# Optimization experiments

Measured on AMD Instinct MI355X. Metric: run time of the kernel, lower is better.

## Reference

```python
import jax, jax.numpy as jnp
import numpy as np

B, T, N, D = 4, 16, 1024, 128
LN_EPS = 1e-5


def setup_inputs() -> dict:
    key = jax.random.key(0)
    k1, k2, k3 = jax.random.split(key, 3)
    X = jax.random.normal(k1, (B, T, N, D), dtype=jnp.float32)
    # normalized adjacency (dense, values in [0,1))
    A = jax.random.uniform(k2, (N, N), dtype=jnp.float32)
    # GCN linear weight (torch nn.Linear, bias=False): out = x @ W.T
    W = jax.random.normal(k3, (D, D), dtype=jnp.float32) / np.sqrt(D)
    gamma = jnp.ones((D,), dtype=jnp.float32)
    beta = jnp.zeros((D,), dtype=jnp.float32)
    return {"X": X, "A": A, "W": W, "gamma": gamma, "beta": beta}


def reference(X, A, W, gamma, beta):
    d = X.shape[-1]
    inv_sqrt_d_a = np.float32(1.0 / np.sqrt(d + 1e-8))  # score scale
    inv_sqrt_d_b = np.float32(1.0 / np.sqrt(d + 1e-9))  # output scale
    # dynamic attention-like scores over nodes: (b,T,N,N)
    scores = jnp.einsum('btnd,btmd->btnm', X, X)
    St = jax.nn.softmax(scores, axis=-1) * inv_sqrt_d_a  # dropout p=0 => identity
    Aeff = A * St                                        # adjacency-masked attention
    # GCN: relu((Aeff @ X) @ W.T)
    h = jnp.einsum('btnm,btmd->btnd', Aeff, X)
    h = jax.nn.relu(h @ W.T) * inv_sqrt_d_b
    # LayerNorm over last dim
    mu = jnp.mean(h, axis=-1, keepdims=True)
    var = jnp.mean(jnp.square(h - mu), axis=-1, keepdims=True)
    h = (h - mu) * jax.lax.rsqrt(var + LN_EPS) * gamma + beta
    # residual
    return h + X
```

## Files before the change

### kernel.cpp

```cpp
#include <hip/hip_runtime.h>


#define NNODES 1024
#define DDIM   128
#define BROWS  128
#define WROWS  16
#define MC     64
#define NCHUNK (NNODES / MC)
#define THREADS 512

#define CA 0.08838834764831845f
#define CB 0.08838834764831845f
#define LN_EPS 1e-5f

typedef __attribute__((ext_vector_type(8))) short bf16x8;
typedef __attribute__((ext_vector_type(4))) float f32x4;
typedef __attribute__((ext_vector_type(2))) unsigned int u32x2;

#define STILE(s) (64*(s))

#define XB0_OFF 0
#define XB1_OFF 8192
#define P_OFF   16384
#define P_S     72
#define H_S     136
#define SM_TOT  25600

#define TRREAD16(T, AP)                                                     \
  asm volatile(                                                             \
    "ds_read_b64_tr_b16 %0, %16 offset:0\n\t"                               \
    "ds_read_b64_tr_b16 %1, %16 offset:128\n\t"                             \
    "ds_read_b64_tr_b16 %2, %16 offset:2048\n\t"                            \
    "ds_read_b64_tr_b16 %3, %16 offset:2176\n\t"                            \
    "ds_read_b64_tr_b16 %4, %16 offset:4096\n\t"                            \
    "ds_read_b64_tr_b16 %5, %16 offset:4224\n\t"                            \
    "ds_read_b64_tr_b16 %6, %16 offset:6144\n\t"                            \
    "ds_read_b64_tr_b16 %7, %16 offset:6272\n\t"                            \
    "ds_read_b64_tr_b16 %8, %16 offset:8192\n\t"                            \
    "ds_read_b64_tr_b16 %9, %16 offset:8320\n\t"                            \
    "ds_read_b64_tr_b16 %10, %16 offset:10240\n\t"                          \
    "ds_read_b64_tr_b16 %11, %16 offset:10368\n\t"                          \
    "ds_read_b64_tr_b16 %12, %16 offset:12288\n\t"                          \
    "ds_read_b64_tr_b16 %13, %16 offset:12416\n\t"                          \
    "ds_read_b64_tr_b16 %14, %16 offset:14336\n\t"                          \
    "ds_read_b64_tr_b16 %15, %16 offset:14464\n\t"                          \
    "s_waitcnt lgkmcnt(0)"                                                  \
    : "=&v"(T[0]), "=&v"(T[1]), "=&v"(T[2]), "=&v"(T[3]),                   \
      "=&v"(T[4]), "=&v"(T[5]), "=&v"(T[6]), "=&v"(T[7]),                   \
      "=&v"(T[8]), "=&v"(T[9]), "=&v"(T[10]), "=&v"(T[11]),                 \
      "=&v"(T[12]), "=&v"(T[13]), "=&v"(T[14]), "=&v"(T[15])                \
    : "v"(AP))

__device__ __forceinline__ unsigned short f2bf(float f) {
  unsigned int u = __float_as_uint(f);
  u += 0x7FFFu + ((u >> 16) & 1u);
  return (unsigned short)(u >> 16);
}

__device__ __forceinline__ bf16x8 pack8(float4 a, float4 b) {
  union { bf16x8 v; unsigned short u[8]; } pk;
  pk.u[0] = f2bf(a.x); pk.u[1] = f2bf(a.y); pk.u[2] = f2bf(a.z); pk.u[3] = f2bf(a.w);
  pk.u[4] = f2bf(b.x); pk.u[5] = f2bf(b.y); pk.u[6] = f2bf(b.z); pk.u[7] = f2bf(b.w);
  return pk.v;
}

__global__ __launch_bounds__(THREADS, 4)
void sdgcn_fused(const float* __restrict__ X, const float* __restrict__ A,
                 const float* __restrict__ W, const float* __restrict__ gamma,
                 const float* __restrict__ beta, float* __restrict__ Out) {
  const int bt   = blockIdx.x;
  const int row0 = blockIdx.y * BROWS;
  const int tid  = (int)threadIdx.x;
  const int wid  = tid >> 6;
  const int lane = tid & 63;
  const int c    = lane & 15;
  const int q    = lane >> 4;
  const int c2 = c >> 2, c3 = c & 3, q1 = q & 1, q2 = q >> 1;

  const float* Xbt = X + (size_t)bt * NNODES * DDIM;

  __shared__ __align__(128) unsigned short sm[SM_TOT];
  unsigned short* Pw = sm + P_OFF + wid * (WROWS * P_S);

  const int pswz = 16 * ((c >> 3) & 1);

  bf16x8 qfrag[4];
  float ss = 0.f;
  {
    const float* qrow = Xbt + (size_t)(row0 + wid * WROWS + c) * DDIM;
#pragma unroll
    for (int ds = 0; ds < 4; ++ds) {
      const float* p = qrow + ds * 32 + q * 8;
      float4 a = *(const float4*)p;
      float4 b = *(const float4*)(p + 4);
      ss += a.x*a.x + a.y*a.y + a.z*a.z + a.w*a.w;
      ss += b.x*b.x + b.y*b.y + b.z*b.z + b.w*b.w;
      qfrag[ds] = pack8(a, b);
    }
    ss += __shfl_xor(ss, 16, 64);
    ss += __shfl_xor(ss, 32, 64);
  }

  float z_acc = 0.f;
  f32x4 Ofr[8];
#pragma unroll
  for (int dt = 0; dt < 8; ++dt) Ofr[dt] = (f32x4){0.f, 0.f, 0.f, 0.f};

  const int grow = row0 + wid * WROWS + q * 4;
  const int arow = row0 + wid * WROWS + c;

  const int h4  = tid & 15;
  const int mlo = (tid >> 4) & 3;
  const int sd4 = h4 + 16 * (wid & 1);
  const int mh0 = wid >> 1;

  float4 stg[4];
#pragma unroll
  for (int k = 0; k < 4; ++k)
    stg[k] = *(const float4*)(Xbt + (size_t)(mlo + 4*(mh0 + 4*k)) * DDIM + sd4 * 4);

  for (int ch = 0; ch < NCHUNK; ++ch) {
    const int m0 = ch * MC;
    unsigned short* xb = sm + ((ch & 1) ? XB1_OFF : XB0_OFF);
    const unsigned trb = (unsigned)(size_t)xb + 256u*q + 8u*c;
#pragma unroll
    for (int k = 0; k < 4; ++k) {
      float4 v = stg[k];
      unsigned int lo = (unsigned int)f2bf(v.x) | ((unsigned int)f2bf(v.y) << 16);
      unsigned int hi = (unsigned int)f2bf(v.z) | ((unsigned int)f2bf(v.w) << 16);
      const int s = (sd4 >> 2) * 16 + (mh0 + 4*k);
      *(uint2*)(xb + STILE(s) + 16*mlo + 4*(sd4 & 3)) = make_uint2(lo, hi);
    }
    __syncthreads();
    if (ch + 1 < NCHUNK) {
      const float* nx = Xbt + (size_t)(m0 + MC) * DDIM;
#pragma unroll
      for (int k = 0; k < 4; ++k)
        stg[k] = *(const float4*)(nx + (size_t)(mlo + 4*(mh0 + 4*k)) * DDIM + sd4 * 4);
    }
    float4 av[4];
#pragma unroll
    for (int mt = 0; mt < 4; ++mt)
      av[mt] = *(const float4*)(A + (size_t)arow * NNODES + m0 + mt*16 + 4*q);
    f32x4 S[4];
#pragma unroll
    for (int mt = 0; mt < 4; ++mt) {
      f32x4 acc = (f32x4){0.f, 0.f, 0.f, 0.f};
#pragma unroll
      for (int ds = 0; ds < 4; ++ds) {
        const bf16x8 bf = *(const bf16x8*)(xb + STILE((ds*2 + q2)*16 + mt*4 + c2)
                                              + 16*c3 + 8*q1);
        acc = __builtin_amdgcn_mfma_f32_16x16x32_bf16(bf, qfrag[ds], acc, 0, 0, 0);
      }
      S[mt] = acc;
    }
    float zr = 0.f;
#pragma unroll
    for (int mt = 0; mt < 4; ++mt) {
      float p0 = __expf(S[mt][0] - ss);
      float p1 = __expf(S[mt][1] - ss);
      float p2 = __expf(S[mt][2] - ss);
      float p3 = __expf(S[mt][3] - ss);
      zr += (p0 + p1) + (p2 + p3);
      unsigned int lo = (unsigned int)f2bf(p0 * av[mt].x) | ((unsigned int)f2bf(p1 * av[mt].y) << 16);
      unsigned int hi = (unsigned int)f2bf(p2 * av[mt].z) | ((unsigned int)f2bf(p3 * av[mt].w) << 16);
      *(uint2*)(Pw + c * P_S + ((mt*16 + 4*q) ^ pswz)) = make_uint2(lo, hi);
    }
    z_acc += zr;
#pragma unroll
    for (int ks = 0; ks < 2; ++ks) {
      const bf16x8 pf = *(const bf16x8*)(Pw + c * P_S + ((ks*32 + q*8) ^ pswz));
      u32x2 T[16];
      TRREAD16(T, trb + 1024u*ks);
      __builtin_amdgcn_sched_barrier(0);
#pragma unroll
      for (int dt = 0; dt < 8; ++dt) {
        union { u32x2 d[2]; bf16x8 v; } u;
        u.d[0] = T[2*dt]; u.d[1] = T[2*dt + 1];
        Ofr[dt] = __builtin_amdgcn_mfma_f32_16x16x32_bf16(pf, u.v, Ofr[dt], 0, 0, 0);
      }
    }
  }

  z_acc += __shfl_xor(z_acc, 16, 64);
  z_acc += __shfl_xor(z_acc, 32, 64);
  float zrow[4];
#pragma unroll
  for (int r = 0; r < 4; ++r)
    zrow[r] = __shfl(z_acc, (lane & 48) + ((lane & 48) >> 2) + r, 64);

  __syncthreads();
  unsigned short* Hw = sm + wid * (WROWS * H_S);
#pragma unroll
  for (int r = 0; r < 4; ++r) {
    float rinv = CA / zrow[r];
#pragma unroll
    for (int dt = 0; dt < 8; ++dt)
      Hw[(q*4 + r) * H_S + (((dt*16) ^ (16*(q>>1))) + c)] = f2bf(Ofr[dt][r] * rinv);
  }
  f32x4 G[8];
#pragma unroll
  for (int jt = 0; jt < 8; ++jt) G[jt] = (f32x4){0.f, 0.f, 0.f, 0.f};
#pragma unroll
  for (int ks = 0; ks < 4; ++ks) {
    bf16x8 hf = *(const bf16x8*)(Hw + c * H_S + ((ks*32 + q*8) ^ pswz));
#pragma unroll
    for (int jt = 0; jt < 8; ++jt) {
      const float* wr = W + (size_t)(jt*16 + c) * DDIM + ks*32 + q*8;
      float4 a = *(const float4*)wr;
      float4 b = *(const float4*)(wr + 4);
      bf16x8 wf = pack8(a, b);
      G[jt] = __builtin_amdgcn_mfma_f32_16x16x32_bf16(hf, wf, G[jt], 0, 0, 0);
    }
  }
#pragma unroll
  for (int jt = 0; jt < 8; ++jt) {
#pragma unroll
    for (int r = 0; r < 4; ++r) G[jt][r] = fmaxf(G[jt][r], 0.f) * CB;
  }
  float* Obt = Out + (size_t)bt * NNODES * DDIM;
#pragma unroll
  for (int r = 0; r < 4; ++r) {
    float s1 = 0.f, s2 = 0.f;
#pragma unroll
    for (int jt = 0; jt < 8; ++jt) { float v = G[jt][r]; s1 += v; s2 += v * v; }
#pragma unroll
    for (int off = 1; off < 16; off <<= 1) {
      s1 += __shfl_xor(s1, off, 64);
      s2 += __shfl_xor(s2, off, 64);
    }
    float mu = s1 * (1.f / 128.f);
    float va = s2 * (1.f / 128.f) - mu * mu;
    float rs = rsqrtf(va + LN_EPS);
    const float* xr = Xbt + (size_t)(grow + r) * DDIM;
    float* orow = Obt + (size_t)(grow + r) * DDIM;
#pragma unroll
    for (int jt = 0; jt < 8; ++jt) {
      int col = jt * 16 + c;
      orow[col] = (G[jt][r] - mu) * rs * gamma[col] + beta[col] + xr[col];
    }
  }
}

extern "C" void kernel_launch(void* const* d_in, const int* in_sizes, int n_in,
                              void* d_out, int out_size, void* d_ws, size_t ws_size,
                              hipStream_t stream) {
  const float* X     = (const float*)d_in[0];
  const float* A     = (const float*)d_in[1];
  const float* W     = (const float*)d_in[2];
  const float* gamma = (const float*)d_in[3];
  const float* beta  = (const float*)d_in[4];
  float* Out = (float*)d_out;
  dim3 grid(64, NNODES / BROWS);
  hipLaunchKernelGGL(sdgcn_fused, grid, dim3(THREADS), 0, stream, X, A, W, gamma, beta, Out);
}
```

Baseline: 201.0 us.

## Write next X chunk to LDS during compute and split transposed reads

Moves the bf16 conversion and LDS store of the next X chunk into the current iteration, after the score MFMAs, targeting the other double buffer. This removes the store-then-sync serialization at the top of each chunk, so global-load latency and LDS writes overlap compute. The 16 transposed LDS reads are also split into two batches of 8, interleaved with the PV MFMAs, which lowers register pressure and overlaps loads with math. The cost is more live registers for the staged data across the score phase, and correctness now relies on the single barrier covering the buffer reuse.

After: 175.8 us. 12.6% less time.

```diff
diff --git a/kernel.cpp b/kernel.cpp
--- a/kernel.cpp
+++ b/kernel.cpp
@@ -26,29 +26,19 @@
 #define H_S     136
 #define SM_TOT  25600
 
-#define TRREAD16(T, AP)                                                     \
+#define TRREAD8(T0,T1,T2,T3,T4,T5,T6,T7, AP)                                \
   asm volatile(                                                             \
-    "ds_read_b64_tr_b16 %0, %16 offset:0\n\t"                               \
-    "ds_read_b64_tr_b16 %1, %16 offset:128\n\t"                             \
-    "ds_read_b64_tr_b16 %2, %16 offset:2048\n\t"                            \
-    "ds_read_b64_tr_b16 %3, %16 offset:2176\n\t"                            \
-    "ds_read_b64_tr_b16 %4, %16 offset:4096\n\t"                            \
-    "ds_read_b64_tr_b16 %5, %16 offset:4224\n\t"                            \
-    "ds_read_b64_tr_b16 %6, %16 offset:6144\n\t"                            \
-    "ds_read_b64_tr_b16 %7, %16 offset:6272\n\t"                            \
-    "ds_read_b64_tr_b16 %8, %16 offset:8192\n\t"                            \
-    "ds_read_b64_tr_b16 %9, %16 offset:8320\n\t"                            \
-    "ds_read_b64_tr_b16 %10, %16 offset:10240\n\t"                          \
-    "ds_read_b64_tr_b16 %11, %16 offset:10368\n\t"                          \
-    "ds_read_b64_tr_b16 %12, %16 offset:12288\n\t"                          \
-    "ds_read_b64_tr_b16 %13, %16 offset:12416\n\t"                          \
-    "ds_read_b64_tr_b16 %14, %16 offset:14336\n\t"                          \
-    "ds_read_b64_tr_b16 %15, %16 offset:14464\n\t"                          \
+    "ds_read_b64_tr_b16 %0, %8 offset:0\n\t"                                \
+    "ds_read_b64_tr_b16 %1, %8 offset:128\n\t"                              \
+    "ds_read_b64_tr_b16 %2, %8 offset:2048\n\t"                             \
+    "ds_read_b64_tr_b16 %3, %8 offset:2176\n\t"                             \
+    "ds_read_b64_tr_b16 %4, %8 offset:4096\n\t"                             \
+    "ds_read_b64_tr_b16 %5, %8 offset:4224\n\t"                             \
+    "ds_read_b64_tr_b16 %6, %8 offset:6144\n\t"                             \
+    "ds_read_b64_tr_b16 %7, %8 offset:6272\n\t"                             \
     "s_waitcnt lgkmcnt(0)"                                                  \
-    : "=&v"(T[0]), "=&v"(T[1]), "=&v"(T[2]), "=&v"(T[3]),                   \
-      "=&v"(T[4]), "=&v"(T[5]), "=&v"(T[6]), "=&v"(T[7]),                   \
-      "=&v"(T[8]), "=&v"(T[9]), "=&v"(T[10]), "=&v"(T[11]),                 \
-      "=&v"(T[12]), "=&v"(T[13]), "=&v"(T[14]), "=&v"(T[15])                \
+    : "=&v"(T0), "=&v"(T1), "=&v"(T2), "=&v"(T3),                           \
+      "=&v"(T4), "=&v"(T5), "=&v"(T6), "=&v"(T7)                            \
     : "v"(AP))
 
 __device__ __forceinline__ unsigned short f2bf(float f) {
@@ -62,6 +52,12 @@
   pk.u[0] = f2bf(a.x); pk.u[1] = f2bf(a.y); pk.u[2] = f2bf(a.z); pk.u[3] = f2bf(a.w);
   pk.u[4] = f2bf(b.x); pk.u[5] = f2bf(b.y); pk.u[6] = f2bf(b.z); pk.u[7] = f2bf(b.w);
   return pk.v;
+}
+
+__device__ __forceinline__ bf16x8 joinpair(u32x2 lo, u32x2 hi) {
+  union { u32x2 d[2]; bf16x8 v; } u;
+  u.d[0] = lo; u.d[1] = hi;
+  return u.v;
 }
 
 __global__ __launch_bounds__(THREADS, 4)
@@ -113,25 +109,32 @@
   const int mlo = (tid >> 4) & 3;
   const int sd4 = h4 + 16 * (wid & 1);
   const int mh0 = wid >> 1;
-
-  float4 stg[4];
-#pragma unroll
-  for (int k = 0; k < 4; ++k)
-    stg[k] = *(const float4*)(Xbt + (size_t)(mlo + 4*(mh0 + 4*k)) * DDIM + sd4 * 4);
-
-  for (int ch = 0; ch < NCHUNK; ++ch) {
-    const int m0 = ch * MC;
-    unsigned short* xb = sm + ((ch & 1) ? XB1_OFF : XB0_OFF);
-    const unsigned trb = (unsigned)(size_t)xb + 256u*q + 8u*c;
+  const int sst = (sd4 >> 2) * 16 + mh0;
+  const int sof = 16*mlo + 4*(sd4 & 3);
+
+  {
+    float4 stg[4];
+#pragma unroll
+    for (int k = 0; k < 4; ++k)
+      stg[k] = *(const float4*)(Xbt + (size_t)(mlo + 4*(mh0 + 4*k)) * DDIM + sd4 * 4);
 #pragma unroll
     for (int k = 0; k < 4; ++k) {
       float4 v = stg[k];
       unsigned int lo = (unsigned int)f2bf(v.x) | ((unsigned int)f2bf(v.y) << 16);
       unsigned int hi = (unsigned int)f2bf(v.z) | ((unsigned int)f2bf(v.w) << 16);
-      const int s = (sd4 >> 2) * 16 + (mh0 + 4*k);
-      *(uint2*)(xb + STILE(s) + 16*mlo + 4*(sd4 & 3)) = make_uint2(lo, hi);
-    }
+      *(uint2*)(sm + XB0_OFF + STILE(sst + 4*k) + sof) = make_uint2(lo, hi);
+    }
+  }
+
+  for (int ch = 0; ch < NCHUNK; ++ch) {
+    const int m0 = ch * MC;
+    unsigned short* xb  = sm + ((ch & 1) ? XB1_OFF : XB0_OFF);
+    unsigned short* xbn = sm + ((ch & 1) ? XB0_OFF : XB1_OFF);
+    const unsigned trb = (unsigned)(size_t)xb + 256u*q + 8u*c;
+
     __syncthreads();
+
+    float4 stg[4];
     if (ch + 1 < NCHUNK) {
       const float* nx = Xbt + (size_t)(m0 + MC) * DDIM;
 #pragma unroll
@@ -153,6 +156,15 @@
         acc = __builtin_amdgcn_mfma_f32_16x16x32_bf16(bf, qfrag[ds], acc, 0, 0, 0);
       }
       S[mt] = acc;
+    }
+    if (ch + 1 < NCHUNK) {
+#pragma unroll
+      for (int k = 0; k < 4; ++k) {
+        float4 v = stg[k];
+        unsigned int lo = (unsigned int)f2bf(v.x) | ((unsigned int)f2bf(v.y) << 16);
+        unsigned int hi = (unsigned int)f2bf(v.z) | ((unsigned int)f2bf(v.w) << 16);
+        *(uint2*)(xbn + STILE(sst + 4*k) + sof) = make_uint2(lo, hi);
+      }
     }
     float zr = 0.f;
 #pragma unroll
@@ -170,15 +182,17 @@
 #pragma unroll
     for (int ks = 0; ks < 2; ++ks) {
       const bf16x8 pf = *(const bf16x8*)(Pw + c * P_S + ((ks*32 + q*8) ^ pswz));
-      u32x2 T[16];
-      TRREAD16(T, trb + 1024u*ks);
-      __builtin_amdgcn_sched_barrier(0);
-#pragma unroll
-      for (int dt = 0; dt < 8; ++dt) {
-        union { u32x2 d[2]; bf16x8 v; } u;
-        u.d[0] = T[2*dt]; u.d[1] = T[2*dt + 1];
-        Ofr[dt] = __builtin_amdgcn_mfma_f32_16x16x32_bf16(pf, u.v, Ofr[dt], 0, 0, 0);
-      }
+      u32x2 t0, t1, t2, t3, t4, t5, t6, t7;
+      TRREAD8(t0, t1, t2, t3, t4, t5, t6, t7, trb + 1024u*ks);
+      Ofr[0] = __builtin_amdgcn_mfma_f32_16x16x32_bf16(pf, joinpair(t0, t1), Ofr[0], 0, 0, 0);
+      Ofr[1] = __builtin_amdgcn_mfma_f32_16x16x32_bf16(pf, joinpair(t2, t3), Ofr[1], 0, 0, 0);
+      Ofr[2] = __builtin_amdgcn_mfma_f32_16x16x32_bf16(pf, joinpair(t4, t5), Ofr[2], 0, 0, 0);
+      Ofr[3] = __builtin_amdgcn_mfma_f32_16x16x32_bf16(pf, joinpair(t6, t7), Ofr[3], 0, 0, 0);
+      TRREAD8(t0, t1, t2, t3, t4, t5, t6, t7, trb + 1024u*ks + 8192u);
+      Ofr[4] = __builtin_amdgcn_mfma_f32_16x16x32_bf16(pf, joinpair(t0, t1), Ofr[4], 0, 0, 0);
+      Ofr[5] = __builtin_amdgcn_mfma_f32_16x16x32_bf16(pf, joinpair(t2, t3), Ofr[5], 0, 0, 0);
+      Ofr[6] = __builtin_amdgcn_mfma_f32_16x16x32_bf16(pf, joinpair(t4, t5), Ofr[6], 0, 0, 0);
+      Ofr[7] = __builtin_amdgcn_mfma_f32_16x16x32_bf16(pf, joinpair(t6, t7), Ofr[7], 0, 0, 0);
     }
   }
 
```
